# Optimization experiments

Measured on AMD Instinct MI355X. Metric: run time of the kernel, lower is better.

The kernel has to match this reference:

```python
import jax, jax.numpy as jnp
import numpy as np

M0 = 0.05
R = 2
SIZE = (64, 64)
LIMS = ((1.0, 64.0), (1.0, 64.0))


def _make_grid():
    # torch make_grid: linspace reversed on H axis, forward on W axis,
    # cartesian_prod(ys, xs) then column-swap -> points are (x, y)
    H, W = SIZE
    ys = jnp.linspace(LIMS[0][1], LIMS[0][0], H)
    xs = jnp.linspace(LIMS[1][0], LIMS[1][1], W)
    yy, xx = jnp.meshgrid(ys, xs, indexing="ij")
    return jnp.stack([xx.ravel(), yy.ravel()], axis=-1)  # [HW, 2]


def _pairwise_dist(grid):
    # [HW, HW] euclidean distance (r == 2 path of cal_dist)
    d2 = jnp.sum((grid[:, None, :] - grid[None, :, :]) ** 2, axis=-1)
    return jnp.sqrt(d2)


def setup_inputs() -> dict:
    key = jax.random.key(0)
    x = jax.random.uniform(key, (4, 3, 64, 64), dtype=jnp.float32)
    return {"x": x}


def reference(x):
    B, C, H, W = x.shape
    HW = H * W
    weight = x.reshape(B, C, HW)                      # [B, C, HW]
    bound = M0 * jnp.sum(weight, -1, keepdims=True)   # [B, C, 1]

    # data-dependent max_k (torch does this eagerly via .item(); keep eager)
    sw_cumsum = jnp.cumsum(jnp.sort(weight, -1), -1)  # [B, C, HW]
    max_k = int(jnp.max(jnp.sum(sw_cumsum < bound, -1))) + 1
    max_k = min(max_k, HW)

    # KNN over the fixed grid distance matrix
    dist = _pairwise_dist(_make_grid())               # [HW, HW]
    neg_d, knn_index = jax.lax.top_k(-dist, max_k)    # smallest-k, ascending
    knn_dist = -neg_d                                 # [HW, max_k]

    # weighted DTM using KNN (r == 2)
    knn_weight = weight[:, :, knn_index]              # [B, C, HW, max_k]
    cum_w = jnp.cumsum(knn_weight, -1)                # [B, C, HW, max_k]
    bound4 = bound[..., None]                         # [B, C, 1, 1]
    # searchsorted(left): first idx with cum_w >= bound == count of cum_w < bound
    k = jnp.sum(cum_w < bound4, -1, keepdims=True)    # [B, C, HW, 1]
    k = jnp.clip(k, 0, max_k - 1)
    r_dist = (knn_dist ** 2)[None, None]              # [1, 1, HW, max_k]
    cum_dist = jnp.cumsum(r_dist * knn_weight, -1)
    val = jnp.take_along_axis(cum_dist + r_dist * (bound4 - cum_w), k, axis=-1)
    dtm = jnp.sqrt(val[..., 0] / bound)               # [B, C, HW]
    return dtm.reshape(B, C, H, W)
```

## Files before the change

kernel.cpp:

```cpp
#include <hip/hip_runtime.h>
#include <stdint.h>


#define HW     4096
#define NOFF   16129
#define NPAD   16384
#define NBIN   8192
#define NCHUNK 16

struct Ent { uint32_t off; float d2; };
struct Tables { Ent e[NPAD]; };

constexpr Tables make_tables() {
    Tables t{};
    int cnt[NBIN] = {};
    for (int idx = 0; idx < NOFF; ++idx) {
        int di = idx / 127 - 63, dj = idx % 127 - 63;
        cnt[di * di + dj * dj]++;
    }
    int run = 0;
    for (int b = 0; b < NBIN; ++b) { int c = cnt[b]; cnt[b] = run; run += c; }
    for (int idx = 0; idx < NOFF; ++idx) {
        int di = idx / 127 - 63, dj = idx % 127 - 63;
        int d2 = di * di + dj * dj;
        int pos = cnt[d2]++;
        t.e[pos].off = (uint32_t)((di + 63) << 7) | (uint32_t)(dj + 63);
        t.e[pos].d2  = (float)d2;
    }
    for (int p = NOFF; p < NPAD; ++p) {
        t.e[p].off = 127u;
        t.e[p].d2  = 0.0f;
    }
    return t;
}

__device__ const Tables g_t = make_tables();

__global__ __launch_bounds__(1024) void dtm_kernel(const float* __restrict__ x,
                                                   float* __restrict__ out) {
    __shared__ float  w[HW];
    __shared__ float2 summ[NCHUNK][64];
    __shared__ float  red[16];

    int bc   = blockIdx.x >> 6;
    int pi   = blockIdx.x & 63;
    int tid  = threadIdx.x;
    int lane = tid & 63;
    int wv   = tid >> 6;

    const float4* xb = (const float4*)(x + (size_t)bc * HW);
    float4 v = xb[tid];
    ((float4*)w)[tid] = v;
    float s = (v.x + v.y) + (v.z + v.w);
    #pragma unroll
    for (int off = 32; off >= 1; off >>= 1) s += __shfl_down(s, off, 64);
    if (lane == 0) red[wv] = s;
    __syncthreads();

    {
        int base = __builtin_amdgcn_readfirstlane(wv) << 6;
        float mass = 0.f, d2m = 0.f;
        #pragma unroll 8
        for (int k = 0; k < 64; ++k) {
            Ent e = g_t.e[base + k];
            int qi = pi + (int)((e.off >> 7) & 127u) - 63;
            int qj = lane + (int)(e.off & 127u) - 63;
            bool ok = ((unsigned)qi < 64u) & ((unsigned)qj < 64u);
            float wq = w[(((unsigned)qi & 63u) << 6) | ((unsigned)qj & 63u)];
            wq = ok ? wq : 0.f;
            mass += wq;
            d2m = fmaf(e.d2, wq, d2m);
        }
        summ[wv][lane] = make_float2(mass, d2m);
    }
    __syncthreads();
    if (wv != 0) return;

    float bound = 0.f;
    #pragma unroll
    for (int i = 0; i < 16; ++i) bound += red[i];
    bound *= 0.05f;

    float rem = bound, cumd = 0.f;
    int cstar = NCHUNK;
    bool found = false;
    #pragma unroll
    for (int c = 0; c < NCHUNK; ++c) {
        float2 p = summ[c][lane];
        bool cross = (!found) & (p.x >= rem);
        bool adv   = (!found) & (!cross);
        cstar = cross ? c : cstar;
        found = found | cross;
        rem   = adv ? rem - p.x : rem;
        cumd  = adv ? cumd + p.y : cumd;
    }

    float val = 0.f;
    bool done = false;
    int pos = cstar << 6;
    #pragma unroll 8
    for (int k = 0; k < 64; ++k) {
        Ent e = g_t.e[pos + k];
        int qi = pi + (int)((e.off >> 7) & 127u) - 63;
        int qj = lane + (int)(e.off & 127u) - 63;
        bool ok = ((unsigned)qi < 64u) & ((unsigned)qj < 64u) & (!done);
        float wq = w[(((unsigned)qi & 63u) << 6) | ((unsigned)qj & 63u)];
        wq = ok ? wq : 0.f;
        bool cross = (!done) & (wq >= rem);
        float cv = fmaf(e.d2, rem, cumd);
        val  = cross ? cv : val;
        done = done | cross;
        cumd = fmaf(e.d2, wq, cumd);
        rem  = rem - wq;
    }
    pos += 64;

    while (__any(!done)) {
        int idx = pos < NPAD ? pos : NPAD - 1;
        Ent e = g_t.e[idx];
        int qi = pi + (int)((e.off >> 7) & 127u) - 63;
        int qj = lane + (int)(e.off & 127u) - 63;
        bool ok = ((unsigned)qi < 64u) & ((unsigned)qj < 64u) & (!done);
        float wq = w[(((unsigned)qi & 63u) << 6) | ((unsigned)qj & 63u)];
        wq = ok ? wq : 0.f;
        bool cross = (!done) & ((wq >= rem) | (pos >= NPAD));
        float cv = fmaf(e.d2, rem, cumd);
        val  = cross ? cv : val;
        done = done | cross;
        cumd = fmaf(e.d2, wq, cumd);
        rem  = rem - wq;
        pos++;
    }

    out[(size_t)bc * HW + (pi << 6) + lane] = sqrtf(val / bound);
}

extern "C" void kernel_launch(void* const* d_in, const int* in_sizes, int n_in,
                              void* d_out, int out_size, void* d_ws, size_t ws_size,
                              hipStream_t stream) {
    const float* x = (const float*)d_in[0];
    float* out = (float*)d_out;
    int BC = in_sizes[0] / HW;
    dtm_kernel<<<BC * 64, 1024, 0, stream>>>(x, out);
}
```

Before: 71.05 us.

## Use zero-padded shared weight rows and lane-broadcast table entries to drop bounds checks

Stores the 64x64 weights in a zero-padded shared buffer (192-wide rows), so column-out-of-range reads return zero and the column bounds check goes away. Each thread loads one table entry into a register, and the chunk-sum loop broadcasts it with readlane instead of reading global memory per iteration. The row check becomes a uniform branch. The first 1024 entries are also staged transposed in shared memory for the refinement pass. This raises shared memory use and adds an extra barrier plus zero-fill stores.

```diff
diff --git a/kernel.cpp b/kernel.cpp
--- a/kernel.cpp
+++ b/kernel.cpp
@@ -7,6 +7,8 @@
 #define NPAD   16384
 #define NBIN   8192
 #define NCHUNK 16
+#define WPS    192
+#define WPN    (64 * WPS)
 
 struct Ent { uint32_t off; float d2; };
 struct Tables { Ent e[NPAD]; };
@@ -36,10 +38,11 @@
 
 __device__ const Tables g_t = make_tables();
 
-__global__ __launch_bounds__(1024) void dtm_kernel(const float* __restrict__ x,
-                                                   float* __restrict__ out) {
-    __shared__ float  w[HW];
+__global__ __launch_bounds__(1024, 8) void dtm_kernel(const float* __restrict__ x,
+                                                      float* __restrict__ out) {
+    __shared__ float  wp[WPN];
     __shared__ float2 summ[NCHUNK][64];
+    __shared__ uint2  eb[1024];
     __shared__ float  red[16];
 
     int bc   = blockIdx.x >> 6;
@@ -48,31 +51,44 @@
     int lane = tid & 63;
     int wv   = tid >> 6;
 
+    float4 z = make_float4(0.f, 0.f, 0.f, 0.f);
+    float4* wp4 = (float4*)wp;
+    wp4[tid] = z; wp4[tid + 1024] = z; wp4[tid + 2048] = z;
+
     const float4* xb = (const float4*)(x + (size_t)bc * HW);
     float4 v = xb[tid];
-    ((float4*)w)[tid] = v;
+    const uint2* gt = (const uint2*)g_t.e;
+    uint2 ev  = gt[tid];
+    uint2 ebv = gt[((tid & 15) << 6) | (tid >> 4)];
+
+    __syncthreads();
+
+    {
+        int row = tid >> 4;
+        int col = (tid & 15) << 2;
+        *(float4*)&wp[row * WPS + 64 + col] = v;
+    }
+    eb[tid] = ebv;
     float s = (v.x + v.y) + (v.z + v.w);
     #pragma unroll
     for (int off = 32; off >= 1; off >>= 1) s += __shfl_down(s, off, 64);
     if (lane == 0) red[wv] = s;
     __syncthreads();
 
-    {
-        int base = __builtin_amdgcn_readfirstlane(wv) << 6;
-        float mass = 0.f, d2m = 0.f;
-        #pragma unroll 8
-        for (int k = 0; k < 64; ++k) {
-            Ent e = g_t.e[base + k];
-            int qi = pi + (int)((e.off >> 7) & 127u) - 63;
-            int qj = lane + (int)(e.off & 127u) - 63;
-            bool ok = ((unsigned)qi < 64u) & ((unsigned)qj < 64u);
-            float wq = w[(((unsigned)qi & 63u) << 6) | ((unsigned)qj & 63u)];
-            wq = ok ? wq : 0.f;
+    float mass = 0.f, d2m = 0.f;
+    #pragma unroll 16
+    for (int k = 0; k < 64; ++k) {
+        uint32_t eo = (uint32_t)__builtin_amdgcn_readlane((int)ev.x, k);
+        int qi = pi + (int)((eo >> 7) & 127u) - 63;
+        if ((unsigned)qi < 64u) {
+            float d2 = __uint_as_float(
+                (uint32_t)__builtin_amdgcn_readlane(__float_as_int(0.f) | (int)ev.y, k));
+            float wq = wp[qi * WPS + 64 + ((int)(eo & 127u) - 63) + lane];
             mass += wq;
-            d2m = fmaf(e.d2, wq, d2m);
+            d2m = fmaf(d2, wq, d2m);
         }
-        summ[wv][lane] = make_float2(mass, d2m);
     }
+    summ[wv][lane] = make_float2(mass, d2m);
     __syncthreads();
     if (wv != 0) return;
 
@@ -82,53 +98,52 @@
     bound *= 0.05f;
 
     float rem = bound, cumd = 0.f;
-    int cstar = NCHUNK;
+    int cstar = 15;
     bool found = false;
     #pragma unroll
-    for (int c = 0; c < NCHUNK; ++c) {
+    for (int c = 0; c < 15; ++c) {
         float2 p = summ[c][lane];
-        bool cross = (!found) & (p.x >= rem);
-        bool adv   = (!found) & (!cross);
+        bool cross = (!found) && (p.x >= rem);
         cstar = cross ? c : cstar;
-        found = found | cross;
-        rem   = adv ? rem - p.x : rem;
-        cumd  = adv ? cumd + p.y : cumd;
+        bool adv = (!found) && (!cross);
+        rem  = adv ? rem - p.x : rem;
+        cumd = adv ? cumd + p.y : cumd;
+        found = found || cross;
     }
 
     float val = 0.f;
     bool done = false;
-    int pos = cstar << 6;
     #pragma unroll 8
     for (int k = 0; k < 64; ++k) {
-        Ent e = g_t.e[pos + k];
-        int qi = pi + (int)((e.off >> 7) & 127u) - 63;
-        int qj = lane + (int)(e.off & 127u) - 63;
-        bool ok = ((unsigned)qi < 64u) & ((unsigned)qj < 64u) & (!done);
-        float wq = w[(((unsigned)qi & 63u) << 6) | ((unsigned)qj & 63u)];
+        uint2 e = eb[(k << 4) | cstar];
+        int qi = pi + (int)((e.x >> 7) & 127u) - 63;
+        int jj = 64 + (int)(e.x & 127u) - 63 + lane;
+        float wq = wp[((qi & 63) * WPS) + jj];
+        bool ok = ((unsigned)qi < 64u) && !done;
         wq = ok ? wq : 0.f;
-        bool cross = (!done) & (wq >= rem);
-        float cv = fmaf(e.d2, rem, cumd);
-        val  = cross ? cv : val;
-        done = done | cross;
-        cumd = fmaf(e.d2, wq, cumd);
-        rem  = rem - wq;
+        float d2 = __uint_as_float(e.y);
+        bool cross = (!done) && (wq >= rem);
+        val  = cross ? fmaf(d2, rem, cumd) : val;
+        done = done || cross;
+        cumd = fmaf(d2, wq, cumd);
+        rem -= wq;
     }
-    pos += 64;
+    int pos = (cstar << 6) + 64;
 
     while (__any(!done)) {
         int idx = pos < NPAD ? pos : NPAD - 1;
-        Ent e = g_t.e[idx];
-        int qi = pi + (int)((e.off >> 7) & 127u) - 63;
-        int qj = lane + (int)(e.off & 127u) - 63;
-        bool ok = ((unsigned)qi < 64u) & ((unsigned)qj < 64u) & (!done);
-        float wq = w[(((unsigned)qi & 63u) << 6) | ((unsigned)qj & 63u)];
+        uint2 e = gt[idx];
+        int qi = pi + (int)((e.x >> 7) & 127u) - 63;
+        int jj = 64 + (int)(e.x & 127u) - 63 + lane;
+        float wq = wp[((qi & 63) * WPS) + jj];
+        bool ok = ((unsigned)qi < 64u) && !done;
         wq = ok ? wq : 0.f;
-        bool cross = (!done) & ((wq >= rem) | (pos >= NPAD));
-        float cv = fmaf(e.d2, rem, cumd);
-        val  = cross ? cv : val;
-        done = done | cross;
-        cumd = fmaf(e.d2, wq, cumd);
-        rem  = rem - wq;
+        float d2 = __uint_as_float(e.y);
+        bool cross = (!done) && ((wq >= rem) || (pos >= NPAD));
+        val  = cross ? fmaf(d2, rem, cumd) : val;
+        done = done || cross;
+        cumd = fmaf(d2, wq, cumd);
+        rem -= wq;
         pos++;
     }
 
```

Result: slower. 74.37 us (+4.7%).
